# Kernel optimization log

Hardware: AMD Instinct MI355X
Metric: run time of the kernel (lower is better)

The kernel has to match this reference:

```python
import jax, jax.numpy as jnp
import numpy as np

NUM_THINGS = 80
NUM_STUFF = 53
IGNORE_CLASS = NUM_THINGS + NUM_STUFF  # 133, default ignore_class == -1 path
OVERLAP_THR = 0.5
STUFF_AREA_THR = 4096
THING_CONF_THR = 0.5
INSTANCE_OFFSET = 1000
NUM_SEM_CLASSES = NUM_THINGS + NUM_STUFF + 1  # label range [0, 133]


def setup_inputs() -> dict:
    key = jax.random.key(0)
    k1, k2, k3, k4 = jax.random.split(key, 4)
    B, N, H, W = 2, 100, 800, 1344
    ins_masks = jax.random.randint(k1, (B, N, H, W), 0, 2).astype(jnp.bool_)
    ins_scores = jax.random.uniform(k2, (B, N), dtype=jnp.float32)
    ins_class_ids = jax.random.randint(k3, (B, N), 0, NUM_THINGS, dtype=jnp.int32)
    sem_masks = jax.random.randint(k4, (B, H, W), 0, NUM_SEM_CLASSES, dtype=jnp.int32)
    return {"ins_masks": ins_masks, "ins_scores": ins_scores,
            "ins_class_ids": ins_class_ids, "sem_masks": sem_masks}


def _combine_segms(masks, scores, cls_ids, sem):
    # masks: [N,H,W] bool, scores: [N] f32, cls_ids: [N] i32, sem: [H,W] i32
    order = jnp.argsort(-scores)  # descending by score
    masks = masks[order]
    scores = scores[order]
    cls_ids = cls_ids[order]

    def step(carry, xs):
        pan, iid = carry  # pan: [H,W] i32, iid: i32 (next instance id)
        m, s, c = xs
        area = jnp.sum(m).astype(jnp.float32)
        inter = jnp.sum(m & (pan != 0)).astype(jnp.float32)
        keep = (s >= THING_CONF_THR) & (area > 0) & (inter <= OVERLAP_THR * area)
        write = keep & m & (pan == 0)  # only overwrite free pixels
        pan = jnp.where(write, c + iid * INSTANCE_OFFSET, pan)
        iid = iid + keep.astype(jnp.int32)
        return (pan, iid), None

    pan0 = jnp.zeros(masks.shape[1:], dtype=jnp.int32)
    (pan, _), _ = jax.lax.scan(step, (pan0, jnp.int32(1)), (masks, scores, cls_ids))

    # Stuff fusion: pixels claimed by things become ignore class, then any
    # remaining semantic class with area >= thr (and not ignored) is written.
    sem2 = jnp.where(pan > 0, IGNORE_CLASS, sem)
    counts = jnp.zeros((NUM_SEM_CLASSES,), jnp.int32).at[sem2.ravel()].add(1)
    valid = counts >= STUFF_AREA_THR
    valid = valid.at[IGNORE_CLASS].set(False)
    pan = jnp.where(valid[sem2], sem2 + NUM_THINGS, pan)
    return pan


def reference(ins_masks, ins_scores, ins_class_ids, sem_masks):
    # Batched greedy panoptic fusion -> [B,H,W] int32
    return jax.vmap(_combine_segms)(ins_masks, ins_scores, ins_class_ids, sem_masks)
```

## Files before the change

kernel.cpp:

```cpp
#include <hip/hip_runtime.h>
#include <stdint.h>

#define NB 2
#define NN 100
#define HWP (800*1344)
#define GCH 10
#define NCHMAX 8
#define NKEY (1<<(GCH+1))
#define CBIT (1u<<GCH)
#define NSEM 134
#define IGN 133
#define THR 1024
#define BPI 128
#define GRID (NB*BPI)
#define PPB (HWP/BPI)
#define GPX 8
#define NG (PPB/GPX)
#define NCPY 8

struct WS {
  unsigned hist8[NCPY][NCHMAX][NB][NKEY];
  unsigned counts[NB][NSEM];
  int      iid[NB][NN];
  int      order[NB][NN];
  float    score_s[NB][NN];
  int      cls_s[NB][NN];
  unsigned kcAfter[NCHMAX][NB];
  unsigned Mcnt[NB];
  unsigned flag;
};
#define ZW (NCPY*NCHMAX*NB*NKEY + NB*NSEM + NB*NN)

__device__ __forceinline__ unsigned u8x8_to_bits(uint2 v) {
  unsigned lo = (((v.x & 0x01010101u) * 0x01020408u) >> 24) & 0xFu;
  unsigned hi = (((v.y & 0x01010101u) * 0x01020408u) >> 24) & 0xFu;
  return lo | (hi << 4);
}

__device__ __forceinline__ unsigned load8(const void* __restrict__ masks,
                                          size_t eo, int mode_u8) {
  if (mode_u8) return u8x8_to_bits(*(const uint2*)((const uint8_t*)masks + eo));
  const uint4* mp = (const uint4*)((const int*)masks + eo);
  uint4 a = mp[0], b = mp[1];
  return (a.x & 1u) | ((a.y & 1u) << 1) | ((a.z & 1u) << 2) | ((a.w & 1u) << 3) |
         ((b.x & 1u) << 4) | ((b.y & 1u) << 5) | ((b.z & 1u) << 6) | ((b.w & 1u) << 7);
}

__global__ __launch_bounds__(THR) void k0_setup(
    const void* __restrict__ masks, const float* __restrict__ scores,
    const int* __restrict__ cls, WS* __restrict__ ws, uint8_t* __restrict__ owner) {
  const int t = threadIdx.x, gid = blockIdx.x;
  unsigned* zp = &ws->hist8[0][0][0][0];
  for (unsigned i = (unsigned)gid * THR + t; i < (unsigned)ZW; i += (unsigned)GRID * THR)
    zp[i] = 0;
  uint4* ow = (uint4*)owner;
  const unsigned nw = (unsigned)(NB * HWP / 16);
  for (unsigned i = (unsigned)gid * THR + t; i < nw; i += (unsigned)GRID * THR)
    ow[i] = make_uint4(~0u, ~0u, ~0u, ~0u);
  if (gid == 0) {
    __shared__ float ss[NB * NN];
    __shared__ unsigned shDet;
    const unsigned* mw = (const unsigned*)masks;
    unsigned any = 0;
    for (int i = t; i < 4096; i += THR) any |= (mw[i] > 1u) ? 1u : 0u;
    if (t == 0) shDet = 0;
    if (t < NB * NN) ss[t] = scores[t];
    if (t < NB) ws->Mcnt[t] = 0;
    __syncthreads();
    if (any) atomicOr(&shDet, 1u);
    __syncthreads();
    if (t == 0) ws->flag = shDet;
    if (t < NB * NN) {
      int bb = t / NN, i = t % NN;
      float s = ss[bb * NN + i];
      if (s >= 0.5f) {
        int r = 0;
        for (int j = 0; j < NN; ++j) {
          float sj = ss[bb * NN + j];
          if (sj >= 0.5f && (sj > s || (sj == s && j < i))) r++;
        }
        ws->order[bb][r]   = i;
        ws->score_s[bb][r] = s;
        ws->cls_s[bb][r]   = cls[bb * NN + i];
        atomicAdd(&ws->Mcnt[bb], 1u);
      }
    }
  }
}

__global__ __launch_bounds__(THR, 4) void k_chunk(
    const void* __restrict__ masks, const int* __restrict__ sem,
    WS* __restrict__ ws, uint8_t* __restrict__ owner,
    int c, int doHist, int doCounts) {
  __shared__ unsigned lh[NKEY];
  __shared__ int midx[GCH];
  __shared__ int pmidx[GCH];
  __shared__ unsigned sh_kmask;
  const int t = threadIdx.x, gid = blockIdx.x;
  const int b = gid / BPI, bx = gid % BPI;
  const int M = (int)ws->Mcnt[b];
  int Lp = (c > 0) ? (M - (c - 1) * GCH) : 0; if (Lp > GCH) Lp = GCH;
  int Lc = doHist ? (M - c * GCH) : 0;        if (Lc > GCH) Lc = GCH;
  if (!doCounts && Lp <= 0 && Lc <= 0) return;

  unsigned h[32];
  if (Lp > 0) {
    if (t < GCH) pmidx[t] = ws->order[b][(c - 1) * GCH + t];
    for (int i = t; i < NKEY; i += THR) {
      unsigned v = 0;
      #pragma unroll
      for (int s8 = 0; s8 < NCPY; ++s8) v += ws->hist8[s8][c - 1][b][i];
      lh[i] = v;
    }
    __syncthreads();
    if (t < 64) {
      #pragma unroll
      for (int j = 0; j < 32; ++j) h[j] = lh[t + (j << 6)];
    }
    __syncthreads();
  }

  if (Lc > 0) {
    for (int i = t; i < NKEY; i += THR) lh[i] = 0;
    if (t < GCH) midx[t] = ws->order[b][(t < Lc) ? (c * GCH + t) : (c * GCH)];
  } else if (doCounts) {
    for (int i = t; i < NSEM; i += THR) lh[i] = 0;
  }

  if (Lp > 0) {
    if (t < 64) {
      unsigned km = 0;
      unsigned kc = (c >= 2) ? ws->kcAfter[c - 2][b] : 0u;
      for (int g = 0; g < Lp; ++g) {
        unsigned sel = km & ((1u << g) - 1u);
        unsigned area = 0, inter = 0;
        #pragma unroll
        for (int j = 0; j < 32; ++j) {
          unsigned i = (unsigned)t + ((unsigned)j << 6);
          if ((i >> g) & 1u) {
            area += h[j];
            if ((i >> GCH) | (i & sel)) inter += h[j];
          }
        }
        #pragma unroll
        for (int off = 32; off; off >>= 1) {
          area  += __shfl_xor(area, off);
          inter += __shfl_xor(inter, off);
        }
        float s = ws->score_s[b][(c - 1) * GCH + g];
        bool keep = (s >= 0.5f) && (area > 0u) && (2u * inter <= area);
        if (keep) {
          km |= 1u << g; kc += 1u;
          if (t == 0 && bx == 0) ws->iid[b][(c - 1) * GCH + g] = (int)kc;
        }
      }
      if (t == 0) { sh_kmask = km; if (bx == 0) ws->kcAfter[c - 1][b] = kc; }
    }
  } else if (t == 0) sh_kmask = 0;
  __syncthreads();

  const unsigned kmask = sh_kmask;
  const int mode_u8 = (int)ws->flag;
  const size_t sbase = (size_t)b * HWP + (size_t)bx * PPB;
  int midx_r[GCH], pmidx_r[GCH];
  if (Lc > 0) {
    #pragma unroll
    for (int g = 0; g < GCH; ++g) midx_r[g] = __builtin_amdgcn_readfirstlane(midx[g]);
  }
  if (kmask) {
    #pragma unroll
    for (int g = 0; g < GCH; ++g) pmidx_r[g] = __builtin_amdgcn_readfirstlane(pmidx[g]);
  }

  for (int s = 0; s < 2; ++s) {
    int gr = s * THR + t;
    if (gr >= NG) break;
    const int l0 = gr * GPX;
    const size_t off = (size_t)bx * PPB + l0;
    unsigned w2[2];
    unsigned free8;
    if (c <= 1) {
      w2[0] = ~0u; w2[1] = ~0u; free8 = 0xFFu;
    } else {
      uint2 ov = *(const uint2*)(owner + sbase + l0);
      w2[0] = ov.x; w2[1] = ov.y;
      free8 = 0;
      #pragma unroll
      for (int k = 0; k < GPX; ++k)
        if (((w2[k >> 2] >> ((k & 3) * 8)) & 0xFFu) == 0xFFu) free8 |= 1u << k;
    }
    if (kmask) {
      unsigned rem = kmask;
      bool chg = false;
      while (rem && free8) {
        int g = __builtin_ctz(rem); rem &= rem - 1u;
        unsigned b8 = load8(masks, (size_t)(b * NN + pmidx_r[g]) * HWP + off, mode_u8);
        unsigned take = b8 & free8;
        if (take) {
          unsigned rank = (unsigned)((c - 1) * GCH + g);
          #pragma unroll
          for (int k = 0; k < GPX; ++k)
            if ((take >> k) & 1u)
              w2[k >> 2] = (w2[k >> 2] & ~(0xFFu << ((k & 3) * 8))) |
                           (rank << ((k & 3) * 8));
          free8 &= ~take; chg = true;
        }
      }
      if (chg) *(uint2*)(owner + sbase + l0) = make_uint2(w2[0], w2[1]);
    }
    const unsigned claimed8 = ~free8 & 0xFFu;

    if (Lc > 0) {
      unsigned key[GPX];
      #pragma unroll
      for (int k = 0; k < GPX; ++k)
        key[k] = ((claimed8 >> k) & 1u) << GCH;
      if (mode_u8) {
        #pragma unroll
        for (int g = 0; g < GCH; ++g) {
          unsigned b8 = u8x8_to_bits(*(const uint2*)((const uint8_t*)masks +
              (size_t)(b * NN + midx_r[g]) * HWP + off));
          #pragma unroll
          for (int k = 0; k < GPX; ++k) key[k] |= ((b8 >> k) & 1u) << g;
        }
      } else {
        #pragma unroll 2
        for (int g = 0; g < GCH; ++g) {
          unsigned b8 = load8(masks, (size_t)(b * NN + midx_r[g]) * HWP + off, 0);
          #pragma unroll
          for (int k = 0; k < GPX; ++k) key[k] |= ((b8 >> k) & 1u) << g;
        }
      }
      const unsigned lm = (Lc >= GCH) ? (CBIT | (CBIT - 1u))
                                      : (CBIT | ((1u << Lc) - 1u));
      #pragma unroll
      for (int k = 0; k < GPX; ++k)
        atomicAdd(&lh[key[k] & lm], 1u);
    }
    if (doCounts) {
      const uint4* sp = (const uint4*)(sem + sbase + l0);
      uint4 sv0 = sp[0], sv1 = sp[1];
      unsigned sarr[8] = {sv0.x, sv0.y, sv0.z, sv0.w, sv1.x, sv1.y, sv1.z, sv1.w};
      #pragma unroll
      for (int k = 0; k < GPX; ++k)
        if (((free8 >> k) & 1u) && sarr[k] != (unsigned)IGN)
          atomicAdd(&lh[sarr[k]], 1u);
    }
  }
  __syncthreads();
  if (Lc > 0) {
    unsigned* hp = &ws->hist8[bx & (NCPY - 1)][c][b][0];
    for (int i = t; i < NKEY; i += THR) {
      unsigned v = lh[i];
      if (v) atomicAdd(&hp[i], v);
    }
  } else if (doCounts) {
    for (int i = t; i < NSEM; i += THR) {
      unsigned v = lh[i];
      if (v) atomicAdd(&ws->counts[b][i], v);
    }
  }
}

__global__ __launch_bounds__(THR) void k_writepan(
    const int* __restrict__ sem, const uint8_t* __restrict__ owner,
    const WS* __restrict__ ws, int* __restrict__ out) {
  __shared__ int pval[NN];
  __shared__ int sval[NSEM];
  const int t = threadIdx.x, gid = blockIdx.x;
  const int b = gid / BPI, bx = gid % BPI;
  const size_t sbase = (size_t)b * HWP + (size_t)bx * PPB;
  if (t < NN)  pval[t] = ws->cls_s[b][t] + ws->iid[b][t] * 1000;
  if (t < NSEM) sval[t] = (t != IGN && ws->counts[b][t] >= 4096u) ? (t + 80) : 0;
  __syncthreads();
  for (int s = 0; s < 2; ++s) {
    int gr = s * THR + t;
    if (gr >= NG) break;
    int l0 = gr * GPX;
    uint2 ov = *(const uint2*)(owner + sbase + l0);
    unsigned w2[2] = {ov.x, ov.y};
    const uint4* sp = (const uint4*)(sem + sbase + l0);
    uint4 sv0 = sp[0], sv1 = sp[1];
    unsigned sarr[8] = {sv0.x, sv0.y, sv0.z, sv0.w, sv1.x, sv1.y, sv1.z, sv1.w};
    int4* op = (int4*)(out + sbase + l0);
    #pragma unroll
    for (int q = 0; q < 2; ++q) {
      int res[4];
      #pragma unroll
      for (int j = 0; j < 4; ++j) {
        int k = q * 4 + j;
        unsigned by = (w2[k >> 2] >> ((k & 3) * 8)) & 0xFFu;
        res[j] = (by != 0xFFu) ? pval[by] : sval[sarr[k]];
      }
      op[q] = make_int4(res[0], res[1], res[2], res[3]);
    }
  }
}

extern "C" void kernel_launch(void* const* d_in, const int* in_sizes, int n_in,
                              void* d_out, int out_size, void* d_ws, size_t ws_size,
                              hipStream_t stream) {
  const void*  masks  = d_in[0];
  const float* scores = (const float*)d_in[1];
  const int*   cls    = (const int*)d_in[2];
  const int*   sem    = (const int*)d_in[3];
  int* out = (int*)d_out;

  uint8_t* base = (uint8_t*)d_ws;
  WS* ws = (WS*)base;
  size_t off = (sizeof(WS) + 255) & ~(size_t)255;
  uint8_t* owner = base + off;

  hipLaunchKernelGGL(k0_setup, dim3(GRID), dim3(THR), 0, stream,
                     masks, scores, cls, ws, owner);
  for (int c = 0; c < NCHMAX; ++c)
    hipLaunchKernelGGL(k_chunk, dim3(GRID), dim3(THR), 0, stream,
                       masks, sem, ws, owner, c, 1, 0);
  hipLaunchKernelGGL(k_chunk, dim3(GRID), dim3(THR), 0, stream,
                     masks, sem, ws, owner, NCHMAX, 0, 1);
  hipLaunchKernelGGL(k_writepan, dim3(GRID), dim3(THR), 0, stream,
                     sem, owner, ws, out);
}
```

Baseline: 182.9 us.

## Precompute per-pixel 64-bit mask membership words and drive greedy chunks from them

A new first pass reads every kept instance mask once and writes a 64-bit membership bitmask per pixel, while building the histogram for the first chunk. Later chunk passes and the final write read only these words to form histogram keys, the claimed state and the owner. The owner is taken as the lowest kept bit, which replaces the byte owner array and removes repeated mask reads. The trade-off is 8 bytes of extra workspace traffic per pixel on every pass, a single histogram copy with more atomic contention instead of eight, and a hard cap of 64 instances above the score threshold.

```diff
diff --git a/kernel.cpp b/kernel.cpp
--- a/kernel.cpp
+++ b/kernel.cpp
@@ -4,10 +4,10 @@
 #define NB 2
 #define NN 100
 #define HWP (800*1344)
-#define GCH 10
-#define NCHMAX 8
-#define NKEY (1<<(GCH+1))
-#define CBIT (1u<<GCH)
+#define G 10
+#define NCH 7
+#define NKEY (1<<(G+1))
+#define CBIT (1u<<G)
 #define NSEM 134
 #define IGN 133
 #define THR 1024
@@ -16,20 +16,21 @@
 #define PPB (HWP/BPI)
 #define GPX 8
 #define NG (PPB/GPX)
-#define NCPY 8
+#define MCAP 64
 
 struct WS {
-  unsigned hist8[NCPY][NCHMAX][NB][NKEY];
+  unsigned hist[NCH][NB][NKEY];
   unsigned counts[NB][NSEM];
   int      iid[NB][NN];
+  unsigned kmaskArr[NCH][NB];
+  unsigned kcAfter[NCH][NB];
   int      order[NB][NN];
   float    score_s[NB][NN];
   int      cls_s[NB][NN];
-  unsigned kcAfter[NCHMAX][NB];
   unsigned Mcnt[NB];
   unsigned flag;
 };
-#define ZW (NCPY*NCHMAX*NB*NKEY + NB*NSEM + NB*NN)
+#define ZW (NCH*NB*NKEY + NB*NSEM + NB*NN + NCH*NB*2)
 
 __device__ __forceinline__ unsigned u8x8_to_bits(uint2 v) {
   unsigned lo = (((v.x & 0x01010101u) * 0x01020408u) >> 24) & 0xFu;
@@ -48,15 +49,11 @@
 
 __global__ __launch_bounds__(THR) void k0_setup(
     const void* __restrict__ masks, const float* __restrict__ scores,
-    const int* __restrict__ cls, WS* __restrict__ ws, uint8_t* __restrict__ owner) {
+    const int* __restrict__ cls, WS* __restrict__ ws) {
   const int t = threadIdx.x, gid = blockIdx.x;
-  unsigned* zp = &ws->hist8[0][0][0][0];
+  unsigned* zp = &ws->hist[0][0][0];
   for (unsigned i = (unsigned)gid * THR + t; i < (unsigned)ZW; i += (unsigned)GRID * THR)
     zp[i] = 0;
-  uint4* ow = (uint4*)owner;
-  const unsigned nw = (unsigned)(NB * HWP / 16);
-  for (unsigned i = (unsigned)gid * THR + t; i < nw; i += (unsigned)GRID * THR)
-    ow[i] = make_uint4(~0u, ~0u, ~0u, ~0u);
   if (gid == 0) {
     __shared__ float ss[NB * NN];
     __shared__ unsigned shDet;
@@ -88,30 +85,73 @@
   }
 }
 
+__global__ __launch_bounds__(THR, 4) void k_passA(
+    const void* __restrict__ masks, WS* __restrict__ ws,
+    unsigned long long* __restrict__ w1) {
+  __shared__ unsigned lh[NKEY];
+  __shared__ int midx[MCAP];
+  const int t = threadIdx.x, gid = blockIdx.x;
+  const int b = gid / BPI, bx = gid % BPI;
+  int M = (int)ws->Mcnt[b]; if (M > MCAP) M = MCAP;
+  for (int i = t; i < NKEY; i += THR) lh[i] = 0;
+  if (t < MCAP) midx[t] = ws->order[b][t < M ? t : 0];
+  __syncthreads();
+  const int mode_u8 = (int)ws->flag;
+  const size_t sb = (size_t)bx * PPB;
+  for (int s = 0; s < 2; ++s) {
+    int gr = s * THR + t;
+    if (gr >= NG) break;
+    const int l0 = gr * GPX;
+    const size_t off = sb + l0;
+    unsigned long long w[GPX];
+    #pragma unroll
+    for (int k = 0; k < GPX; ++k) w[k] = 0;
+    for (int g0 = 0; g0 < M; g0 += 8) {
+      int n = M - g0; if (n > 8) n = 8;
+      int mi[8];
+      #pragma unroll
+      for (int u = 0; u < 8; ++u)
+        mi[u] = __builtin_amdgcn_readfirstlane(midx[g0 + (u < n ? u : 0)]);
+      #pragma unroll
+      for (int u = 0; u < 8; ++u) {
+        if (u < n) {
+          unsigned b8 = load8(masks, (size_t)(b * NN + mi[u]) * HWP + off, mode_u8);
+          #pragma unroll
+          for (int k = 0; k < GPX; ++k)
+            w[k] |= (unsigned long long)((b8 >> k) & 1u) << (g0 + u);
+        }
+      }
+    }
+    unsigned long long* wp = w1 + (size_t)b * HWP + off;
+    #pragma unroll
+    for (int k = 0; k < GPX; ++k) wp[k] = w[k];
+    #pragma unroll
+    for (int k = 0; k < GPX; ++k)
+      atomicAdd(&lh[(unsigned)(w[k] & (unsigned long long)(CBIT - 1u))], 1u);
+  }
+  __syncthreads();
+  for (int i = t; i < NKEY; i += THR) {
+    unsigned v = lh[i];
+    if (v) atomicAdd(&ws->hist[0][b][i], v);
+  }
+}
+
 __global__ __launch_bounds__(THR, 4) void k_chunk(
-    const void* __restrict__ masks, const int* __restrict__ sem,
-    WS* __restrict__ ws, uint8_t* __restrict__ owner,
-    int c, int doHist, int doCounts) {
+    const int* __restrict__ sem, WS* __restrict__ ws,
+    const unsigned long long* __restrict__ w1, int c, int doCounts) {
   __shared__ unsigned lh[NKEY];
-  __shared__ int midx[GCH];
-  __shared__ int pmidx[GCH];
   __shared__ unsigned sh_kmask;
   const int t = threadIdx.x, gid = blockIdx.x;
   const int b = gid / BPI, bx = gid % BPI;
-  const int M = (int)ws->Mcnt[b];
-  int Lp = (c > 0) ? (M - (c - 1) * GCH) : 0; if (Lp > GCH) Lp = GCH;
-  int Lc = doHist ? (M - c * GCH) : 0;        if (Lc > GCH) Lc = GCH;
+  int M = (int)ws->Mcnt[b]; if (M > MCAP) M = MCAP;
+  int Lp = M - (c - 1) * G; if (Lp > G) Lp = G;
+  int Lc = (c < NCH) ? (M - c * G) : 0; if (Lc > G) Lc = G;
+  if (Lc < 0) Lc = 0;
   if (!doCounts && Lp <= 0 && Lc <= 0) return;
 
   unsigned h[32];
   if (Lp > 0) {
-    if (t < GCH) pmidx[t] = ws->order[b][(c - 1) * GCH + t];
-    for (int i = t; i < NKEY; i += THR) {
-      unsigned v = 0;
-      #pragma unroll
-      for (int s8 = 0; s8 < NCPY; ++s8) v += ws->hist8[s8][c - 1][b][i];
-      lh[i] = v;
-    }
+    for (int i = t; i < NKEY; i += THR) lh[i] = ws->hist[c - 1][b][i];
     __syncthreads();
     if (t < 64) {
       #pragma unroll
@@ -119,14 +159,8 @@
     }
     __syncthreads();
   }
-
-  if (Lc > 0) {
-    for (int i = t; i < NKEY; i += THR) lh[i] = 0;
-    if (t < GCH) midx[t] = ws->order[b][(t < Lc) ? (c * GCH + t) : (c * GCH)];
-  } else if (doCounts) {
-    for (int i = t; i < NSEM; i += THR) lh[i] = 0;
-  }
-
+  if (Lc > 0) { for (int i = t; i < NKEY; i += THR) lh[i] = 0; }
+  else if (doCounts) { for (int i = t; i < NSEM; i += THR) lh[i] = 0; }
   if (Lp > 0) {
     if (t < 64) {
       unsigned km = 0;
@@ -139,7 +173,7 @@
           unsigned i = (unsigned)t + ((unsigned)j << 6);
           if ((i >> g) & 1u) {
             area += h[j];
-            if ((i >> GCH) | (i & sel)) inter += h[j];
+            if ((i >> G) | (i & sel)) inter += h[j];
           }
         }
         #pragma unroll
@@ -147,112 +181,62 @@
           area  += __shfl_xor(area, off);
           inter += __shfl_xor(inter, off);
         }
-        float s = ws->score_s[b][(c - 1) * GCH + g];
+        float s = ws->score_s[b][(c - 1) * G + g];
         bool keep = (s >= 0.5f) && (area > 0u) && (2u * inter <= area);
         if (keep) {
           km |= 1u << g; kc += 1u;
-          if (t == 0 && bx == 0) ws->iid[b][(c - 1) * GCH + g] = (int)kc;
-        }
-      }
-      if (t == 0) { sh_kmask = km; if (bx == 0) ws->kcAfter[c - 1][b] = kc; }
+          if (t == 0 && bx == 0) ws->iid[b][(c - 1) * G + g] = (int)kc;
+        }
+      }
+      if (t == 0) {
+        sh_kmask = km;
+        ws->kmaskArr[c - 1][b] = km;
+        if (bx == 0) ws->kcAfter[c - 1][b] = kc;
+      }
     }
   } else if (t == 0) sh_kmask = 0;
   __syncthreads();
 
-  const unsigned kmask = sh_kmask;
-  const int mode_u8 = (int)ws->flag;
-  const size_t sbase = (size_t)b * HWP + (size_t)bx * PPB;
-  int midx_r[GCH], pmidx_r[GCH];
-  if (Lc > 0) {
-    #pragma unroll
-    for (int g = 0; g < GCH; ++g) midx_r[g] = __builtin_amdgcn_readfirstlane(midx[g]);
-  }
-  if (kmask) {
-    #pragma unroll
-    for (int g = 0; g < GCH; ++g) pmidx_r[g] = __builtin_amdgcn_readfirstlane(pmidx[g]);
-  }
-
+  if (Lc <= 0 && !doCounts) return;
+
+  unsigned long long keptPrev =
+      (unsigned long long)sh_kmask << ((c - 1) * G);
+  for (int j = 0; j < c - 1; ++j)
+    keptPrev |= (unsigned long long)ws->kmaskArr[j][b] << (j * G);
+
+  const size_t base = (size_t)b * HWP + (size_t)bx * PPB;
+  const int sh = (c < NCH) ? c * G : 0;
   for (int s = 0; s < 2; ++s) {
     int gr = s * THR + t;
     if (gr >= NG) break;
     const int l0 = gr * GPX;
-    const size_t off = (size_t)bx * PPB + l0;
-    unsigned w2[2];
-    unsigned free8;
-    if (c <= 1) {
-      w2[0] = ~0u; w2[1] = ~0u; free8 = 0xFFu;
-    } else {
-      uint2 ov = *(const uint2*)(owner + sbase + l0);
-      w2[0] = ov.x; w2[1] = ov.y;
-      free8 = 0;
-      #pragma unroll
-      for (int k = 0; k < GPX; ++k)
-        if (((w2[k >> 2] >> ((k & 3) * 8)) & 0xFFu) == 0xFFu) free8 |= 1u << k;
-    }
-    if (kmask) {
-      unsigned rem = kmask;
-      bool chg = false;
-      while (rem && free8) {
-        int g = __builtin_ctz(rem); rem &= rem - 1u;
-        unsigned b8 = load8(masks, (size_t)(b * NN + pmidx_r[g]) * HWP + off, mode_u8);
-        unsigned take = b8 & free8;
-        if (take) {
-          unsigned rank = (unsigned)((c - 1) * GCH + g);
-          #pragma unroll
-          for (int k = 0; k < GPX; ++k)
-            if ((take >> k) & 1u)
-              w2[k >> 2] = (w2[k >> 2] & ~(0xFFu << ((k & 3) * 8))) |
-                           (rank << ((k & 3) * 8));
-          free8 &= ~take; chg = true;
-        }
-      }
-      if (chg) *(uint2*)(owner + sbase + l0) = make_uint2(w2[0], w2[1]);
-    }
-    const unsigned claimed8 = ~free8 & 0xFFu;
-
+    const unsigned long long* wp = w1 + base + l0;
+    unsigned long long w[GPX];
+    #pragma unroll
+    for (int k = 0; k < GPX; ++k) w[k] = wp[k];
     if (Lc > 0) {
-      unsigned key[GPX];
-      #pragma unroll
-      for (int k = 0; k < GPX; ++k)
-        key[k] = ((claimed8 >> k) & 1u) << GCH;
-      if (mode_u8) {
-        #pragma unroll
-        for (int g = 0; g < GCH; ++g) {
-          unsigned b8 = u8x8_to_bits(*(const uint2*)((const uint8_t*)masks +
-              (size_t)(b * NN + midx_r[g]) * HWP + off));
-          #pragma unroll
-          for (int k = 0; k < GPX; ++k) key[k] |= ((b8 >> k) & 1u) << g;
-        }
-      } else {
-        #pragma unroll 2
-        for (int g = 0; g < GCH; ++g) {
-          unsigned b8 = load8(masks, (size_t)(b * NN + midx_r[g]) * HWP + off, 0);
-          #pragma unroll
-          for (int k = 0; k < GPX; ++k) key[k] |= ((b8 >> k) & 1u) << g;
-        }
-      }
-      const unsigned lm = (Lc >= GCH) ? (CBIT | (CBIT - 1u))
-                                      : (CBIT | ((1u << Lc) - 1u));
-      #pragma unroll
-      for (int k = 0; k < GPX; ++k)
-        atomicAdd(&lh[key[k] & lm], 1u);
+      #pragma unroll
+      for (int k = 0; k < GPX; ++k) {
+        unsigned key = (unsigned)((w[k] >> sh) & (unsigned long long)(CBIT - 1u));
+        if (w[k] & keptPrev) key |= CBIT;
+        atomicAdd(&lh[key], 1u);
+      }
     }
     if (doCounts) {
-      const uint4* sp = (const uint4*)(sem + sbase + l0);
+      const uint4* sp = (const uint4*)(sem + base + l0);
       uint4 sv0 = sp[0], sv1 = sp[1];
       unsigned sarr[8] = {sv0.x, sv0.y, sv0.z, sv0.w, sv1.x, sv1.y, sv1.z, sv1.w};
       #pragma unroll
       for (int k = 0; k < GPX; ++k)
-        if (((free8 >> k) & 1u) && sarr[k] != (unsigned)IGN)
+        if (!(w[k] & keptPrev) && sarr[k] != (unsigned)IGN)
           atomicAdd(&lh[sarr[k]], 1u);
     }
   }
   __syncthreads();
   if (Lc > 0) {
-    unsigned* hp = &ws->hist8[bx & (NCPY - 1)][c][b][0];
     for (int i = t; i < NKEY; i += THR) {
       unsigned v = lh[i];
-      if (v) atomicAdd(&hp[i], v);
+      if (v) atomicAdd(&ws->hist[c][b][i], v);
     }
   } else if (doCounts) {
     for (int i = t; i < NSEM; i += THR) {
@@ -263,34 +247,40 @@
 }
 
 __global__ __launch_bounds__(THR) void k_writepan(
-    const int* __restrict__ sem, const uint8_t* __restrict__ owner,
+    const int* __restrict__ sem, const unsigned long long* __restrict__ w1,
     const WS* __restrict__ ws, int* __restrict__ out) {
   __shared__ int pval[NN];
   __shared__ int sval[NSEM];
   const int t = threadIdx.x, gid = blockIdx.x;
   const int b = gid / BPI, bx = gid % BPI;
-  const size_t sbase = (size_t)b * HWP + (size_t)bx * PPB;
+  const size_t base = (size_t)b * HWP + (size_t)bx * PPB;
   if (t < NN)  pval[t] = ws->cls_s[b][t] + ws->iid[b][t] * 1000;
   if (t < NSEM) sval[t] = (t != IGN && ws->counts[b][t] >= 4096u) ? (t + 80) : 0;
   __syncthreads();
+  unsigned long long keptAll = 0;
+  #pragma unroll
+  for (int j = 0; j < NCH; ++j)
+    keptAll |= (unsigned long long)ws->kmaskArr[j][b] << (j * G);
   for (int s = 0; s < 2; ++s) {
     int gr = s * THR + t;
     if (gr >= NG) break;
-    int l0 = gr * GPX;
-    uint2 ov = *(const uint2*)(owner + sbase + l0);
-    unsigned w2[2] = {ov.x, ov.y};
-    const uint4* sp = (const uint4*)(sem + sbase + l0);
+    const int l0 = gr * GPX;
+    const unsigned long long* wp = w1 + base + l0;
+    unsigned long long w[GPX];
+    #pragma unroll
+    for (int k = 0; k < GPX; ++k) w[k] = wp[k];
+    const uint4* sp = (const uint4*)(sem + base + l0);
     uint4 sv0 = sp[0], sv1 = sp[1];
     unsigned sarr[8] = {sv0.x, sv0.y, sv0.z, sv0.w, sv1.x, sv1.y, sv1.z, sv1.w};
-    int4* op = (int4*)(out + sbase + l0);
+    int4* op = (int4*)(out + base + l0);
     #pragma unroll
     for (int q = 0; q < 2; ++q) {
       int res[4];
       #pragma unroll
       for (int j = 0; j < 4; ++j) {
         int k = q * 4 + j;
-        unsigned by = (w2[k >> 2] >> ((k & 3) * 8)) & 0xFFu;
-        res[j] = (by != 0xFFu) ? pval[by] : sval[sarr[k]];
+        unsigned long long hit = w[k] & keptAll;
+        res[j] = hit ? pval[__builtin_ctzll(hit)] : sval[sarr[k]];
       }
       op[q] = make_int4(res[0], res[1], res[2], res[3]);
     }
@@ -309,15 +299,16 @@
   uint8_t* base = (uint8_t*)d_ws;
   WS* ws = (WS*)base;
   size_t off = (sizeof(WS) + 255) & ~(size_t)255;
-  uint8_t* owner = base + off;
+  unsigned long long* w1 = (unsigned long long*)(base + off);
 
   hipLaunchKernelGGL(k0_setup, dim3(GRID), dim3(THR), 0, stream,
-                     masks, scores, cls, ws, owner);
-  for (int c = 0; c < NCHMAX; ++c)
+                     masks, scores, cls, ws);
+  hipLaunchKernelGGL(k_passA, dim3(GRID), dim3(THR), 0, stream, masks, ws, w1);
+  for (int c = 1; c < NCH; ++c)
     hipLaunchKernelGGL(k_chunk, dim3(GRID), dim3(THR), 0, stream,
-                       masks, sem, ws, owner, c, 1, 0);
+                       sem, ws, w1, c, 0);
   hipLaunchKernelGGL(k_chunk, dim3(GRID), dim3(THR), 0, stream,
-                     masks, sem, ws, owner, NCHMAX, 0, 1);
+                     sem, ws, w1, NCH, 1);
   hipLaunchKernelGGL(k_writepan, dim3(GRID), dim3(THR), 0, stream,
-                     sem, owner, ws, out);
-}
+                     sem, w1, ws, out);
+}
```

Result: slower. 201.8 us (+10.3%).
